# Performance work log

Hardware: AMD Instinct MI355X
Metric: run time of the kernel (lower is better)

The kernel has to match this reference:

```python
import jax, jax.numpy as jnp
import numpy as np

B_SZ, L_MAX, T_LEN, D = 512, 48, 128, 300   # sentences, graph slots, tokens, glove_dim
N_A, N_C = 2048, 2048                        # aspect rows, clause rows
H, TOP_K = 4, 96                             # attention heads, top-k over flattened LxL


def setup_inputs() -> dict:
    key = jax.random.key(0)
    ks = jax.random.split(key, 8)
    input_embed = jax.random.normal(ks[0], (B_SZ, T_LEN, D), jnp.float32)
    clause_output = jax.random.normal(ks[1], (N_C, D), jnp.float32)
    batch_aa_mask = (jax.random.uniform(ks[2], (N_A, T_LEN)) < 0.5).astype(jnp.float32)
    aa_graph_length = jax.random.randint(ks[3], (B_SZ,), 1, L_MAX + 1, dtype=jnp.int32)
    # collision-free scatter destinations; maxima hit B_SZ-1 and L_MAX-1 exactly
    map_AA = jnp.arange(N_A, dtype=jnp.int32) % B_SZ
    map_AA_idx = (4 + jnp.arange(N_A, dtype=jnp.int32) // B_SZ).at[-1].set(L_MAX - 1)
    map_AS = jnp.arange(N_C, dtype=jnp.int32) % B_SZ
    map_AS_idx = jnp.arange(N_C, dtype=jnp.int32) // B_SZ
    sc = 1.0 / np.sqrt(D).astype(np.float32)
    Wq = jax.random.normal(ks[4], (D, D), jnp.float32) * sc
    Wk = jax.random.normal(ks[5], (D, D), jnp.float32) * sc
    Wg = jax.random.normal(ks[6], (D, D), jnp.float32) * sc
    bq = jnp.zeros((D,), jnp.float32)
    bk = jnp.zeros((D,), jnp.float32)
    bg = jnp.zeros((D,), jnp.float32)
    return {"input_embed": input_embed, "clause_output": clause_output,
            "batch_aa_mask": batch_aa_mask, "aa_graph_length": aa_graph_length,
            "map_AA": map_AA, "map_AA_idx": map_AA_idx,
            "map_AS": map_AS, "map_AS_idx": map_AS_idx,
            "Wq": Wq, "bq": bq, "Wk": Wk, "bk": bk, "Wg": Wg, "bg": bg}


def reference(input_embed, clause_output, batch_aa_mask, aa_graph_length,
              map_AA, map_AA_idx, map_AS, map_AS_idx, Wq, bq, Wk, bk, Wg, bg):
    B, L = B_SZ, L_MAX
    dk = D // H
    # gather sentence tokens per aspect, masked sum over tokens -> [Na, D]
    aa_embed = jnp.einsum('ntd,nt->nd', input_embed[map_AA], batch_aa_mask)
    # scatter aspect and clause features into the [B, L, D] graph tensor
    inner = jnp.zeros((B, L, D), input_embed.dtype)
    inner = inner.at[map_AA, map_AA_idx].set(aa_embed)
    inner = inner.at[map_AS, map_AS_idx].set(clause_output)
    mask_indi = (jnp.arange(L)[None, :] < aa_graph_length[:, None]).astype(inner.dtype)  # [B,L]
    # attention-based adjacency (scores only, softmax over keys)
    q = (inner @ Wq.T + bq).reshape(B, L, H, dk).transpose(0, 2, 1, 3)
    k = (inner @ Wk.T + bk).reshape(B, L, H, dk).transpose(0, 2, 1, 3)
    scores = jnp.einsum('bhid,bhjd->bhij', q, k) / jnp.sqrt(jnp.asarray(dk, inner.dtype))
    scores = jnp.where(mask_indi[:, None, None, :] == 0, -1e9, scores)
    attn = jax.nn.softmax(scores, axis=-1)                      # [B,H,L,L]
    # average heads, replace diagonal with self-loops, zero padded rows
    adj = attn.mean(axis=1)
    eye = jnp.eye(L, dtype=adj.dtype)
    adj = adj * (1.0 - eye) + eye
    adj = adj * mask_indi[:, :, None]
    # top-k sparsify over flattened adjacency, symmetrize, diag=1, reweight
    flat = adj.reshape(B, L * L)
    kth = jax.lax.top_k(flat, TOP_K)[0][:, -1]                  # [B]
    sel = (flat >= kth[:, None]).astype(adj.dtype).reshape(B, L, L)
    sel = sel + sel.transpose(0, 2, 1)
    sel = sel * (1.0 - eye) + eye
    adj = sel * adj
    # one GCN layer: relu(W(A x) / (rowsum(A)+1))
    denom = adj.sum(axis=-1, keepdims=True) + 1.0
    gcn = jax.nn.relu((jnp.einsum('bij,bjd->bid', adj, inner) @ Wg.T + bg) / denom)
    # gather back to clause rows; keep clause_output where graph has <=1 node
    aa_out = gcn[map_AS, map_AS_idx]                            # [Nc, D]
    need = (aa_graph_length[map_AS] > 1)[:, None]
    return jnp.where(need, aa_out, clause_output)
```

## Files before the change

### kernel.cpp

```cpp
#include <hip/hip_runtime.h>
#include <math.h>

#define B_SZ 512
#define LG 48
#define T_LEN 128
#define DIM 300
#define NA 2048
#define NC 2048
#define NH 4
#define DK 75
#define KTOP 96
#define ACAP 16
#define TM 64
#define TN 64
#define KC 100
#define QKS 608
#define GTM 32
#define GTN 64
#define GKC 60

__global__ __launch_bounds__(256) void build_kernel(
    const int* __restrict__ mapAA, const int* __restrict__ mapAAi,
    int* __restrict__ slot_src, int* __restrict__ acnt, int* __restrict__ alist) {
  int n = blockIdx.x * 256 + threadIdx.x;
  if (n >= NA) return;
  int b = mapAA[n];
  atomicMax(&slot_src[b * LG + mapAAi[n]], n);
  int pos = atomicAdd(&acnt[b], 1);
  if (pos < ACAP) alist[b * ACAP + pos] = n;
}

__global__ __launch_bounds__(256) void aspect_kernel(
    const float* __restrict__ embed, const float* __restrict__ mask,
    const int* __restrict__ acnt, const int* __restrict__ alist,
    float* __restrict__ X) {
  int b = blockIdx.x;
  int na = acnt[b]; if (na > ACAP) na = ACAP;
  if (na == 0) return;
  __shared__ float mLds[ACAP][T_LEN];
  __shared__ float4 eLds[32][DK];
  int tid = threadIdx.x;
  for (int i = tid; i < na * T_LEN; i += 256) {
    int k = i / T_LEN, t = i - k * T_LEN;
    mLds[k][t] = mask[(size_t)alist[b * ACAP + k] * T_LEN + t];
  }
  int nw = na * DK;
  int i0 = tid, i1 = tid + 256;
  int k0 = i0 / DK, d0 = i0 - k0 * DK;
  int k1 = i1 / DK, d1 = i1 - k1 * DK;
  float4 a0 = {0, 0, 0, 0}, a1 = {0, 0, 0, 0};
  const float4* e4 = (const float4*)(embed + (size_t)b * T_LEN * DIM);
  for (int t0 = 0; t0 < T_LEN; t0 += 32) {
    __syncthreads();
    for (int i = tid; i < 32 * DK; i += 256) {
      int t = i / DK, d = i - t * DK;
      eLds[t][d] = e4[(size_t)(t0 + t) * DK + d];
    }
    __syncthreads();
#pragma unroll
    for (int t = 0; t < 32; ++t) {
      if (i0 < nw) {
        float m = mLds[k0][t0 + t]; float4 ev = eLds[t][d0];
        a0.x += m * ev.x; a0.y += m * ev.y; a0.z += m * ev.z; a0.w += m * ev.w;
      }
      if (i1 < nw) {
        float m = mLds[k1][t0 + t]; float4 ev = eLds[t][d1];
        a1.x += m * ev.x; a1.y += m * ev.y; a1.z += m * ev.z; a1.w += m * ev.w;
      }
    }
  }
  if (i0 < nw) ((float4*)(X + (size_t)alist[b * ACAP + k0] * DIM))[d0] = a0;
  if (i1 < nw) ((float4*)(X + (size_t)alist[b * ACAP + k1] * DIM))[d1] = a1;
}

__global__ __launch_bounds__(128) void clause_kernel(
    const float* __restrict__ clause, const int* __restrict__ mapAS,
    const int* __restrict__ mapASi, float* __restrict__ X,
    int* __restrict__ slot_src) {
  int n = blockIdx.x, t = threadIdx.x;
  const float4* src = (const float4*)(clause + (size_t)n * DIM);
  float4* dst = (float4*)(X + (size_t)(NA + n) * DIM);
  if (t < DIM / 4) dst[t] = src[t];
  if (t == 96) atomicMax(&slot_src[mapAS[n] * LG + mapASi[n]], NA + n);
}

__global__ __launch_bounds__(256) void qk_kernel(
    const float* __restrict__ X, const float* __restrict__ Wq,
    const float* __restrict__ bq, const float* __restrict__ Wk,
    const float* __restrict__ bk, float* __restrict__ QK) {
  __shared__ __align__(16) float xs[TM][KC];
  __shared__ __align__(16) float ws[TN][KC];
  int m0 = blockIdx.x * TM, n0 = blockIdx.y * TN;
  int tid = threadIdx.x;
  int ty = tid >> 4;
  int tx = tid & 15;
  float acc[4][4];
#pragma unroll
  for (int a = 0; a < 4; ++a)
#pragma unroll
    for (int c = 0; c < 4; ++c) acc[a][c] = 0.f;

  for (int kc = 0; kc < DIM; kc += KC) {
    __syncthreads();
    for (int i = tid; i < TM * (KC / 4); i += 256) {
      int r = i / (KC / 4), g = i - r * (KC / 4);
      *(float4*)&xs[r][g * 4] =
          *(const float4*)&X[(size_t)(m0 + r) * DIM + kc + g * 4];
    }
    for (int i = tid; i < TN * (KC / 4); i += 256) {
      int c = i / (KC / 4), g = i - c * (KC / 4);
      int col = n0 + c;
      float4 v = {0.f, 0.f, 0.f, 0.f};
      if (col < 2 * DIM) {
        const float* w = (col < DIM) ? (Wq + (size_t)col * DIM)
                                     : (Wk + (size_t)(col - DIM) * DIM);
        v = *(const float4*)&w[kc + g * 4];
      }
      *(float4*)&ws[c][g * 4] = v;
    }
    __syncthreads();
#pragma unroll 5
    for (int kg = 0; kg < KC / 4; ++kg) {
      float4 xv[4], wv[4];
#pragma unroll
      for (int a = 0; a < 4; ++a) xv[a] = *(const float4*)&xs[ty * 4 + a][kg * 4];
#pragma unroll
      for (int c = 0; c < 4; ++c) wv[c] = *(const float4*)&ws[tx + 16 * c][kg * 4];
#pragma unroll
      for (int a = 0; a < 4; ++a)
#pragma unroll
        for (int c = 0; c < 4; ++c)
          acc[a][c] += wv[c].x * xv[a].x + wv[c].y * xv[a].y +
                       wv[c].z * xv[a].z + wv[c].w * xv[a].w;
    }
  }

#pragma unroll
  for (int cc = 0; cc < 4; ++cc) {
    int col = n0 + tx + 16 * cc;
    if (col < 2 * DIM) {
      float bias; int off;
      if (col < DIM) { bias = bq[col]; off = col + col / DK; }
      else { int c2 = col - DIM; bias = bk[c2]; off = 304 + c2 + c2 / DK; }
#pragma unroll
      for (int a = 0; a < 4; ++a)
        QK[(size_t)(m0 + ty * 4 + a) * QKS + off] = acc[a][cc] + bias;
    }
  }
}

__global__ __launch_bounds__(128) void score_kernel(
    const float* __restrict__ QK, const float* __restrict__ bq,
    const float* __restrict__ bk, const int* __restrict__ slot_src,
    const int* __restrict__ aa_len, float* __restrict__ adjh) {
  int b = blockIdx.x, h = blockIdx.y, tid = threadIdx.x;
  int length = aa_len[b];
  if (length > LG) length = LG;
  if (length <= 1) return;

  __shared__ __align__(16) float qh[LG][76], kh[LG][76];
  __shared__ int srcs[LG];
  if (tid < LG) srcs[tid] = slot_src[b * LG + tid];
  __syncthreads();

  for (int i = tid; i < 2 * LG * 19; i += 128) {
    int half = i / (LG * 19);
    int rem = i - half * (LG * 19);
    int r = rem / 19, g = rem - (rem / 19) * 19;
    if (r >= length) continue;
    int src = srcs[r];
    float4 v;
    if (src >= 0) {
      v = *(const float4*)&QK[(size_t)src * QKS + half * 304 + h * 76 + g * 4];
      if (g == 18) v.w = 0.f;
    } else {
      const float* bias = half ? bk : bq;
      int d0 = g * 4;
      v.x = (d0 + 0 < DK) ? bias[h * DK + d0 + 0] : 0.f;
      v.y = (d0 + 1 < DK) ? bias[h * DK + d0 + 1] : 0.f;
      v.z = (d0 + 2 < DK) ? bias[h * DK + d0 + 2] : 0.f;
      v.w = (d0 + 3 < DK) ? bias[h * DK + d0 + 3] : 0.f;
    }
    float* dst = half ? &kh[r][g * 4] : &qh[r][g * 4];
    *(float4*)dst = v;
  }
  __syncthreads();

  const float sdk = sqrtf((float)DK);
  int ti = tid >> 3, tj = tid & 7;
  int i0 = ti * 3, j0 = tj * 6;
  if (i0 < length) {
    float acc[3][6];
#pragma unroll
    for (int a = 0; a < 3; ++a)
#pragma unroll
      for (int c = 0; c < 6; ++c) acc[a][c] = 0.f;
    for (int d4 = 0; d4 < 19; ++d4) {
      float4 qv[3], kv[6];
#pragma unroll
      for (int a = 0; a < 3; ++a) qv[a] = *(const float4*)&qh[i0 + a][d4 * 4];
#pragma unroll
      for (int c = 0; c < 6; ++c) kv[c] = *(const float4*)&kh[j0 + c][d4 * 4];
#pragma unroll
      for (int a = 0; a < 3; ++a)
#pragma unroll
        for (int c = 0; c < 6; ++c)
          acc[a][c] += qv[a].x * kv[c].x + qv[a].y * kv[c].y +
                       qv[a].z * kv[c].z + qv[a].w * kv[c].w;
    }
    float* outp = adjh + ((size_t)(b * NH + h)) * (LG * LG);
#pragma unroll
    for (int a = 0; a < 3; ++a) {
      float p[6];
#pragma unroll
      for (int c = 0; c < 6; ++c)
        p[c] = (j0 + c < length) ? (acc[a][c] / sdk) : -1e9f;
      float mx = p[0];
#pragma unroll
      for (int c = 1; c < 6; ++c) mx = fmaxf(mx, p[c]);
      mx = fmaxf(mx, __shfl_xor(mx, 1));
      mx = fmaxf(mx, __shfl_xor(mx, 2));
      mx = fmaxf(mx, __shfl_xor(mx, 4));
      float rs = 0.f;
#pragma unroll
      for (int c = 0; c < 6; ++c) { p[c] = expf(p[c] - mx); rs += p[c]; }
      rs += __shfl_xor(rs, 1);
      rs += __shfl_xor(rs, 2);
      rs += __shfl_xor(rs, 4);
      if (i0 + a < length) {
#pragma unroll
        for (int c = 0; c < 6; ++c)
          outp[(i0 + a) * LG + j0 + c] = p[c] / rs;
      }
    }
  }
}

__global__ __launch_bounds__(256) void topk_kernel(
    const float* __restrict__ adjh, const float* __restrict__ X,
    const int* __restrict__ slot_src, const int* __restrict__ aa_len,
    float* __restrict__ xout, float* __restrict__ dng, int* __restrict__ mdg) {
  int b = blockIdx.x, tid = threadIdx.x;
  __shared__ float adj[LG][LG + 1];
  __shared__ float coef[4][LG], denomc[4];
  __shared__ int srcs[LG], nlist[LG], flist[LG];
  __shared__ float kthL;
  __shared__ int sh_nneed, sh_nf;

  int length = aa_len[b];
  if (length > LG) length = LG;
  if (tid < LG) srcs[tid] = slot_src[b * LG + tid];
  __syncthreads();

  if (tid < 64) {
    bool isneed = (tid < LG) && (srcs[tid] >= NA);
    unsigned long long nm = __ballot(isneed);
    if (isneed) nlist[__popcll(nm & ((1ull << tid) - 1ull))] = tid;
    bool isf = (tid < LG) && (srcs[tid] >= 0);
    unsigned long long fm = __ballot(isf);
    if (isf) flist[__popcll(fm & ((1ull << tid) - 1ull))] = tid;
    if (tid == 0) { sh_nneed = __popcll(nm); sh_nf = __popcll(fm); }
  }
  __syncthreads();
  int nneed = sh_nneed;
  int nf = sh_nf;

  if (length <= 1) {
    if (tid < nneed) mdg[srcs[nlist[tid]] - NA] = 0;
    return;
  }

  const float* base = adjh + (size_t)b * NH * (LG * LG);
  for (int e = tid; e < LG * LG; e += 256) {
    int i = e / LG, j = e - (e / LG) * LG;
    float v = 0.f;
    if (i < length) {
      for (int h = 0; h < NH; ++h) v += base[h * (LG * LG) + e];
      v *= 0.25f;
    }
    if (i == j) v = (i < length) ? 1.0f : 0.0f;
    adj[i][j] = v;
  }
  __syncthreads();

  if (tid < 64) {
    unsigned int vb[36];
#pragma unroll
    for (int v = 0; v < 36; ++v) {
      int e = v * 64 + tid;
      vb[v] = __float_as_uint(adj[e / LG][e % LG]);
    }
    unsigned int cur = 0u;
    for (int bit = 30; bit >= 0; --bit) {
      unsigned int cand = cur | (1u << bit);
      int c = 0;
#pragma unroll
      for (int v = 0; v < 36; ++v) c += (vb[v] >= cand) ? 1 : 0;
      c += __shfl_xor(c, 32); c += __shfl_xor(c, 16);
      c += __shfl_xor(c, 8);  c += __shfl_xor(c, 4);
      c += __shfl_xor(c, 2);  c += __shfl_xor(c, 1);
      if (c >= KTOP) cur = cand;
    }
    if (tid == 0) kthL = __uint_as_float(cur);
  }
  __syncthreads();
  const float kth = kthL;

  int nc = (nneed > 4) ? 4 : nneed;
  if (tid < nc * LG) {
    int r = tid / LG, j = tid - (tid / LG) * LG;
    int i = nlist[r];
    float aij = adj[i][j];
    float v;
    if (j == i) v = aij;
    else {
      float selv = (aij >= kth ? 1.f : 0.f) + (adj[j][i] >= kth ? 1.f : 0.f);
      v = selv * aij;
    }
    coef[r][j] = v;
  }
  __syncthreads();
  if (tid < nc) {
    float sm = 0.f;
    for (int j = 0; j < LG; ++j) sm += coef[tid][j];
    denomc[tid] = sm + 1.f;
  }
  __syncthreads();
  for (int w = tid; w < nc * (DIM / 4); w += 256) {
    int r = w / (DIM / 4), d4 = w - (w / (DIM / 4)) * (DIM / 4);
    float4 acc = {0.f, 0.f, 0.f, 0.f};
    for (int m = 0; m < nf; ++m) {
      int j = flist[m];
      float a = coef[r][j];
      float4 xv = ((const float4*)(X + (size_t)srcs[j] * DIM))[d4];
      acc.x += a * xv.x; acc.y += a * xv.y;
      acc.z += a * xv.z; acc.w += a * xv.w;
    }
    int n = srcs[nlist[r]] - NA;
    ((float4*)(xout + (size_t)n * DIM))[d4] = acc;
  }
  if (tid < nc) {
    int n = srcs[nlist[tid]] - NA;
    mdg[n] = 1;
    dng[n] = denomc[tid];
  }
}

__global__ __launch_bounds__(256) void gcn_kernel(
    const float* __restrict__ xg, const float* __restrict__ dng,
    const int* __restrict__ mdg, const float* __restrict__ Wg,
    const float* __restrict__ bg, const float* __restrict__ clause,
    float* __restrict__ out) {
  __shared__ __align__(16) float xs[GTM][GKC];
  __shared__ __align__(16) float ws[GTN][GKC];
  int m0 = blockIdx.x * GTM, n0 = blockIdx.y * GTN;
  int tid = threadIdx.x;
  int ty = tid >> 4;
  int tx = tid & 15;
  float acc[2][4];
#pragma unroll
  for (int a = 0; a < 2; ++a)
#pragma unroll
    for (int c = 0; c < 4; ++c) acc[a][c] = 0.f;

  for (int kc = 0; kc < DIM; kc += GKC) {
    __syncthreads();
    for (int i = tid; i < GTM * (GKC / 4); i += 256) {
      int r = i / (GKC / 4), g = i - r * (GKC / 4);
      *(float4*)&xs[r][g * 4] =
          *(const float4*)&xg[(size_t)(m0 + r) * DIM + kc + g * 4];
    }
    for (int i = tid; i < GTN * (GKC / 4); i += 256) {
      int c = i / (GKC / 4), g = i - c * (GKC / 4);
      int col = n0 + c;
      float4 v = {0.f, 0.f, 0.f, 0.f};
      if (col < DIM)
        v = *(const float4*)&Wg[(size_t)col * DIM + kc + g * 4];
      *(float4*)&ws[c][g * 4] = v;
    }
    __syncthreads();
#pragma unroll 5
    for (int kg = 0; kg < GKC / 4; ++kg) {
      float4 xv[2], wv[4];
#pragma unroll
      for (int a = 0; a < 2; ++a) xv[a] = *(const float4*)&xs[ty * 2 + a][kg * 4];
#pragma unroll
      for (int c = 0; c < 4; ++c) wv[c] = *(const float4*)&ws[tx + 16 * c][kg * 4];
#pragma unroll
      for (int a = 0; a < 2; ++a)
#pragma unroll
        for (int c = 0; c < 4; ++c)
          acc[a][c] += wv[c].x * xv[a].x + wv[c].y * xv[a].y +
                       wv[c].z * xv[a].z + wv[c].w * xv[a].w;
    }
  }

  int md[2]; float dn[2];
#pragma unroll
  for (int a = 0; a < 2; ++a) {
    int row = m0 + ty * 2 + a;
    md[a] = mdg[row];
    dn[a] = dng[row];
  }
#pragma unroll
  for (int cc = 0; cc < 4; ++cc) {
    int col = n0 + tx + 16 * cc;
    if (col < DIM) {
      float bgc = bg[col];
#pragma unroll
      for (int a = 0; a < 2; ++a) {
        int row = m0 + ty * 2 + a;
        float v;
        if (md[a]) v = fmaxf((acc[a][cc] + bgc) / dn[a], 0.f);
        else v = clause[(size_t)row * DIM + col];
        out[(size_t)row * DIM + col] = v;
      }
    }
  }
}

extern "C" void kernel_launch(void* const* d_in, const int* in_sizes, int n_in,
                              void* d_out, int out_size, void* d_ws, size_t ws_size,
                              hipStream_t stream) {
  (void)in_sizes; (void)n_in; (void)out_size; (void)ws_size;
  const float* input_embed = (const float*)d_in[0];
  const float* clause      = (const float*)d_in[1];
  const float* aa_mask     = (const float*)d_in[2];
  const int*   aa_len      = (const int*)d_in[3];
  const int*   map_AA      = (const int*)d_in[4];
  const int*   map_AA_idx  = (const int*)d_in[5];
  const int*   map_AS      = (const int*)d_in[6];
  const int*   map_AS_idx  = (const int*)d_in[7];
  const float* Wq = (const float*)d_in[8];
  const float* bq = (const float*)d_in[9];
  const float* Wk = (const float*)d_in[10];
  const float* bk = (const float*)d_in[11];
  const float* Wg = (const float*)d_in[12];
  const float* bg = (const float*)d_in[13];
  float* out = (float*)d_out;

  float* X  = (float*)d_ws;
  float* QK = X + (size_t)(NA + NC) * DIM;
  int* slot_src = (int*)(QK + (size_t)(NA + NC) * QKS);
  int* acnt = slot_src + B_SZ * LG;
  int* alist = acnt + B_SZ;
  float* dng = (float*)alist;
  int* mdg = (int*)(dng + NC);
  float* xg = (float*)(alist + B_SZ * ACAP);
  float* adjh = xg + (size_t)NC * DIM;

  hipMemsetAsync(slot_src, 0xFF, (size_t)B_SZ * LG * sizeof(int), stream);
  hipMemsetAsync(acnt, 0x00, (size_t)B_SZ * sizeof(int), stream);
  build_kernel<<<(NA + 255) / 256, 256, 0, stream>>>(map_AA, map_AA_idx,
                                                     slot_src, acnt, alist);
  clause_kernel<<<NC, 128, 0, stream>>>(clause, map_AS, map_AS_idx, X, slot_src);
  aspect_kernel<<<B_SZ, 256, 0, stream>>>(input_embed, aa_mask, acnt, alist, X);
  dim3 qkgrid((NA + NC) / TM, (2 * DIM + TN - 1) / TN);
  qk_kernel<<<qkgrid, 256, 0, stream>>>(X, Wq, bq, Wk, bk, QK);
  dim3 sgrid(B_SZ, NH);
  score_kernel<<<sgrid, 128, 0, stream>>>(QK, bq, bk, slot_src, aa_len, adjh);
  topk_kernel<<<B_SZ, 256, 0, stream>>>(adjh, X, slot_src, aa_len, xg, dng, mdg);
  dim3 ggrid(NC / GTM, (DIM + GTN - 1) / GTN);
  gcn_kernel<<<ggrid, 256, 0, stream>>>(xg, dng, mdg, Wg, bg, clause, out);
}
```

Measured before the change: 167.8 us.

## Fuse score and top-k kernels, staging only distinct Q/K rows in shared memory

```diff
diff --git a/kernel.cpp b/kernel.cpp
--- a/kernel.cpp
+++ b/kernel.cpp
@@ -18,6 +18,8 @@
 #define GTM 32
 #define GTN 64
 #define GKC 60
+#define FCAP2 12
+#define SSTR 612
 
 __global__ __launch_bounds__(256) void build_kernel(
     const int* __restrict__ mapAA, const int* __restrict__ mapAAi,
@@ -149,101 +151,16 @@
   }
 }
 
-__global__ __launch_bounds__(128) void score_kernel(
-    const float* __restrict__ QK, const float* __restrict__ bq,
-    const float* __restrict__ bk, const int* __restrict__ slot_src,
-    const int* __restrict__ aa_len, float* __restrict__ adjh) {
-  int b = blockIdx.x, h = blockIdx.y, tid = threadIdx.x;
-  int length = aa_len[b];
-  if (length > LG) length = LG;
-  if (length <= 1) return;
-
-  __shared__ __align__(16) float qh[LG][76], kh[LG][76];
-  __shared__ int srcs[LG];
-  if (tid < LG) srcs[tid] = slot_src[b * LG + tid];
-  __syncthreads();
-
-  for (int i = tid; i < 2 * LG * 19; i += 128) {
-    int half = i / (LG * 19);
-    int rem = i - half * (LG * 19);
-    int r = rem / 19, g = rem - (rem / 19) * 19;
-    if (r >= length) continue;
-    int src = srcs[r];
-    float4 v;
-    if (src >= 0) {
-      v = *(const float4*)&QK[(size_t)src * QKS + half * 304 + h * 76 + g * 4];
-      if (g == 18) v.w = 0.f;
-    } else {
-      const float* bias = half ? bk : bq;
-      int d0 = g * 4;
-      v.x = (d0 + 0 < DK) ? bias[h * DK + d0 + 0] : 0.f;
-      v.y = (d0 + 1 < DK) ? bias[h * DK + d0 + 1] : 0.f;
-      v.z = (d0 + 2 < DK) ? bias[h * DK + d0 + 2] : 0.f;
-      v.w = (d0 + 3 < DK) ? bias[h * DK + d0 + 3] : 0.f;
-    }
-    float* dst = half ? &kh[r][g * 4] : &qh[r][g * 4];
-    *(float4*)dst = v;
-  }
-  __syncthreads();
-
-  const float sdk = sqrtf((float)DK);
-  int ti = tid >> 3, tj = tid & 7;
-  int i0 = ti * 3, j0 = tj * 6;
-  if (i0 < length) {
-    float acc[3][6];
-#pragma unroll
-    for (int a = 0; a < 3; ++a)
-#pragma unroll
-      for (int c = 0; c < 6; ++c) acc[a][c] = 0.f;
-    for (int d4 = 0; d4 < 19; ++d4) {
-      float4 qv[3], kv[6];
-#pragma unroll
-      for (int a = 0; a < 3; ++a) qv[a] = *(const float4*)&qh[i0 + a][d4 * 4];
-#pragma unroll
-      for (int c = 0; c < 6; ++c) kv[c] = *(const float4*)&kh[j0 + c][d4 * 4];
-#pragma unroll
-      for (int a = 0; a < 3; ++a)
-#pragma unroll
-        for (int c = 0; c < 6; ++c)
-          acc[a][c] += qv[a].x * kv[c].x + qv[a].y * kv[c].y +
-                       qv[a].z * kv[c].z + qv[a].w * kv[c].w;
-    }
-    float* outp = adjh + ((size_t)(b * NH + h)) * (LG * LG);
-#pragma unroll
-    for (int a = 0; a < 3; ++a) {
-      float p[6];
-#pragma unroll
-      for (int c = 0; c < 6; ++c)
-        p[c] = (j0 + c < length) ? (acc[a][c] / sdk) : -1e9f;
-      float mx = p[0];
-#pragma unroll
-      for (int c = 1; c < 6; ++c) mx = fmaxf(mx, p[c]);
-      mx = fmaxf(mx, __shfl_xor(mx, 1));
-      mx = fmaxf(mx, __shfl_xor(mx, 2));
-      mx = fmaxf(mx, __shfl_xor(mx, 4));
-      float rs = 0.f;
-#pragma unroll
-      for (int c = 0; c < 6; ++c) { p[c] = expf(p[c] - mx); rs += p[c]; }
-      rs += __shfl_xor(rs, 1);
-      rs += __shfl_xor(rs, 2);
-      rs += __shfl_xor(rs, 4);
-      if (i0 + a < length) {
-#pragma unroll
-        for (int c = 0; c < 6; ++c)
-          outp[(i0 + a) * LG + j0 + c] = p[c] / rs;
-      }
-    }
-  }
-}
-
-__global__ __launch_bounds__(256) void topk_kernel(
-    const float* __restrict__ adjh, const float* __restrict__ X,
+__global__ __launch_bounds__(256) void attn2_kernel(
+    const float* __restrict__ QK, const float* __restrict__ X,
+    const float* __restrict__ bq, const float* __restrict__ bk,
     const int* __restrict__ slot_src, const int* __restrict__ aa_len,
     float* __restrict__ xout, float* __restrict__ dng, int* __restrict__ mdg) {
   int b = blockIdx.x, tid = threadIdx.x;
-  __shared__ float adj[LG][LG + 1];
+  __shared__ __align__(16) float staged[FCAP2][SSTR];
+  __shared__ float bufA[LG][LG + 1], bufB[LG][LG + 1];
   __shared__ float coef[4][LG], denomc[4];
-  __shared__ int srcs[LG], nlist[LG], flist[LG];
+  __shared__ int srcs[LG], nlist[LG], flist[LG], qrow[LG];
   __shared__ float kthL;
   __shared__ int sh_nneed, sh_nf;
 
@@ -258,28 +175,120 @@
     if (isneed) nlist[__popcll(nm & ((1ull << tid) - 1ull))] = tid;
     bool isf = (tid < LG) && (srcs[tid] >= 0);
     unsigned long long fm = __ballot(isf);
-    if (isf) flist[__popcll(fm & ((1ull << tid) - 1ull))] = tid;
-    if (tid == 0) { sh_nneed = __popcll(nm); sh_nf = __popcll(fm); }
-  }
-  __syncthreads();
-  int nneed = sh_nneed;
-  int nf = sh_nf;
+    int nf = __popcll(fm);
+    if (nf > FCAP2 - 1) nf = FCAP2 - 1;
+    if (isf) {
+      int c = __popcll(fm & ((1ull << tid) - 1ull));
+      if (c < FCAP2 - 1) flist[c] = tid;
+    }
+    if (tid < LG) {
+      int c = __popcll(fm & ((1ull << tid) - 1ull));
+      qrow[tid] = (isf && c < FCAP2 - 1) ? c : nf;
+    }
+    if (tid == 0) { sh_nneed = __popcll(nm); sh_nf = nf; }
+  }
+  __syncthreads();
+  int nneed = sh_nneed, nf = sh_nf;
 
   if (length <= 1) {
     if (tid < nneed) mdg[srcs[nlist[tid]] - NA] = 0;
     return;
   }
 
-  const float* base = adjh + (size_t)b * NH * (LG * LG);
+  for (int i = tid; i < nf * 152; i += 256) {
+    int m = i / 152, g = i - m * 152;
+    ((float4*)staged[m])[g] =
+        ((const float4*)(QK + (size_t)srcs[flist[m]] * QKS))[g];
+  }
+  for (int j = tid; j < 608; j += 256) {
+    int half = (j >= 304) ? 1 : 0;
+    int jj = j - half * 304;
+    int h = jj / 76, d = jj - h * 76;
+    float v = 0.f;
+    if (d < DK) v = half ? bk[h * DK + d] : bq[h * DK + d];
+    staged[nf][j] = v;
+  }
+  __syncthreads();
+  if (tid < nf * 8) {
+    int m = tid >> 3, p = tid & 7;
+    int pos = (p & 3) * 76 + 75 + ((p >> 2) * 304);
+    staged[m][pos] = 0.f;
+  }
+  __syncthreads();
+
+  const float sdk = sqrtf((float)DK);
+  int grp = tid >> 7;
+  int t = tid & 127;
+  int ti = t >> 3, tj = t & 7;
+  int i0 = ti * 3, j0 = tj * 6;
+  float (*buf)[LG + 1] = grp ? bufB : bufA;
+
+  int qr[3], kr[6];
+#pragma unroll
+  for (int a = 0; a < 3; ++a) qr[a] = qrow[i0 + a];
+#pragma unroll
+  for (int c = 0; c < 6; ++c) kr[c] = qrow[j0 + c];
+
+  for (int it = 0; it < 2; ++it) {
+    int h = grp * 2 + it;
+    if (i0 < length) {
+      float acc[3][6];
+#pragma unroll
+      for (int a = 0; a < 3; ++a)
+#pragma unroll
+        for (int c = 0; c < 6; ++c) acc[a][c] = 0.f;
+      for (int d4 = 0; d4 < 19; ++d4) {
+        float4 qv[3], kv[6];
+#pragma unroll
+        for (int a = 0; a < 3; ++a)
+          qv[a] = *(const float4*)&staged[qr[a]][h * 76 + d4 * 4];
+#pragma unroll
+        for (int c = 0; c < 6; ++c)
+          kv[c] = *(const float4*)&staged[kr[c]][304 + h * 76 + d4 * 4];
+#pragma unroll
+        for (int a = 0; a < 3; ++a)
+#pragma unroll
+          for (int c = 0; c < 6; ++c)
+            acc[a][c] += qv[a].x * kv[c].x + qv[a].y * kv[c].y +
+                         qv[a].z * kv[c].z + qv[a].w * kv[c].w;
+      }
+#pragma unroll
+      for (int a = 0; a < 3; ++a) {
+        float p[6];
+#pragma unroll
+        for (int c = 0; c < 6; ++c)
+          p[c] = (j0 + c < length) ? (acc[a][c] / sdk) : -1e9f;
+        float mx = p[0];
+#pragma unroll
+        for (int c = 1; c < 6; ++c) mx = fmaxf(mx, p[c]);
+        mx = fmaxf(mx, __shfl_xor(mx, 1));
+        mx = fmaxf(mx, __shfl_xor(mx, 2));
+        mx = fmaxf(mx, __shfl_xor(mx, 4));
+        float rs = 0.f;
+#pragma unroll
+        for (int c = 0; c < 6; ++c) { p[c] = expf(p[c] - mx); rs += p[c]; }
+        rs += __shfl_xor(rs, 1);
+        rs += __shfl_xor(rs, 2);
+        rs += __shfl_xor(rs, 4);
+        if (i0 + a < length) {
+#pragma unroll
+          for (int c = 0; c < 6; ++c) {
+            float val = p[c] / rs;
+            if (it == 0) buf[i0 + a][j0 + c] = val;
+            else buf[i0 + a][j0 + c] += val;
+          }
+        }
+      }
+    }
+  }
+  __syncthreads();
+
   for (int e = tid; e < LG * LG; e += 256) {
     int i = e / LG, j = e - (e / LG) * LG;
     float v = 0.f;
-    if (i < length) {
-      for (int h = 0; h < NH; ++h) v += base[h * (LG * LG) + e];
-      v *= 0.25f;
-    }
+    if (i < length) v = (bufA[i][j] + bufB[i][j]) * 0.25f;
     if (i == j) v = (i < length) ? 1.0f : 0.0f;
-    adj[i][j] = v;
+    bufA[i][j] = v;
   }
   __syncthreads();
 
@@ -288,7 +297,7 @@
 #pragma unroll
     for (int v = 0; v < 36; ++v) {
       int e = v * 64 + tid;
-      vb[v] = __float_as_uint(adj[e / LG][e % LG]);
+      vb[v] = __float_as_uint(bufA[e / LG][e % LG]);
     }
     unsigned int cur = 0u;
     for (int bit = 30; bit >= 0; --bit) {
@@ -310,11 +319,11 @@
   if (tid < nc * LG) {
     int r = tid / LG, j = tid - (tid / LG) * LG;
     int i = nlist[r];
-    float aij = adj[i][j];
+    float aij = bufA[i][j];
     float v;
     if (j == i) v = aij;
     else {
-      float selv = (aij >= kth ? 1.f : 0.f) + (adj[j][i] >= kth ? 1.f : 0.f);
+      float selv = (aij >= kth ? 1.f : 0.f) + (bufA[j][i] >= kth ? 1.f : 0.f);
       v = selv * aij;
     }
     coef[r][j] = v;
@@ -447,7 +456,6 @@
   float* dng = (float*)alist;
   int* mdg = (int*)(dng + NC);
   float* xg = (float*)(alist + B_SZ * ACAP);
-  float* adjh = xg + (size_t)NC * DIM;
 
   hipMemsetAsync(slot_src, 0xFF, (size_t)B_SZ * LG * sizeof(int), stream);
   hipMemsetAsync(acnt, 0x00, (size_t)B_SZ * sizeof(int), stream);
@@ -457,9 +465,8 @@
   aspect_kernel<<<B_SZ, 256, 0, stream>>>(input_embed, aa_mask, acnt, alist, X);
   dim3 qkgrid((NA + NC) / TM, (2 * DIM + TN - 1) / TN);
   qk_kernel<<<qkgrid, 256, 0, stream>>>(X, Wq, bq, Wk, bk, QK);
-  dim3 sgrid(B_SZ, NH);
-  score_kernel<<<sgrid, 128, 0, stream>>>(QK, bq, bk, slot_src, aa_len, adjh);
-  topk_kernel<<<B_SZ, 256, 0, stream>>>(adjh, X, slot_src, aa_len, xg, dng, mdg);
+  attn2_kernel<<<B_SZ, 256, 0, stream>>>(QK, X, bq, bk, slot_src, aa_len,
+                                         xg, dng, mdg);
   dim3 ggrid(NC / GTM, (DIM + GTN - 1) / GTN);
   gcn_kernel<<<ggrid, 256, 0, stream>>>(xg, dng, mdg, Wg, bg, clause, out);
 }
```

New measurement: 153.2 us. 1.1x faster.
